# Performance work log

Measured on AMD Instinct MI355X. Metric: run time of the kernel, lower is better.

## Reference

```python
import jax, jax.numpy as jnp
import numpy as np
from jax import lax

B, NMEAS, M, LAYER_NUM = 2048, 128, 256, 10
CLAMP_MIN, CLAMP_MAX = 1e-6, 100.0
EPS_S = 1e-6


def _conv2d(x, w, b):
    y = lax.conv_general_dilated(x, w, (1, 1), 'SAME', dimension_numbers=('NCHW', 'OIHW', 'NCHW'))
    return y + b[None, :, None, None]


def _conv1d(x, w, b):
    y = lax.conv_general_dilated(x, w, (1,), 'SAME', dimension_numbers=('NCH', 'OIH', 'NCH'))
    return y + b[None, :, None]


def setup_inputs():
    key = jax.random.key(0)
    ks = jax.random.split(key, 12)
    s = 1.0 / np.sqrt(2.0 * NMEAS)  # ~unit-norm dictionary columns
    return {
        'Yr': jax.random.normal(ks[0], (B, 1, NMEAS, 1), jnp.float32),
        'Yi': jax.random.normal(ks[1], (B, 1, NMEAS, 1), jnp.float32),
        'Ar': s * jax.random.normal(ks[2], (NMEAS, M), jnp.float32),
        'Ai': s * jax.random.normal(ks[3], (NMEAS, M), jnp.float32),
        'conv1_w': 0.1 * jax.random.normal(ks[4], (32, 2, 3, 3), jnp.float32),
        'conv1_b': jnp.zeros((32,), jnp.float32),
        'conv2_w': 0.1 * jax.random.normal(ks[5], (64, 32, 3, 3), jnp.float32),
        'conv2_b': jnp.zeros((64,), jnp.float32),
        'hc_w': 0.1 * jax.random.normal(ks[6], (LAYER_NUM - 1, 64, 3), jnp.float32),
        'hc_b': jnp.zeros((LAYER_NUM - 1,), jnp.float32),
        'hd_w': 0.1 * jax.random.normal(ks[7], (LAYER_NUM - 1, 64, 3), jnp.float32),
        'hd_b': jnp.zeros((LAYER_NUM - 1,), jnp.float32),
        'hT_w': 0.1 * jax.random.normal(ks[8], (LAYER_NUM, 64, 3), jnp.float32),
        'hT_b': jnp.zeros((LAYER_NUM,), jnp.float32),
        'a0': jnp.asarray(1.0, jnp.float32),
        'b0': jnp.asarray(1.0, jnp.float32),
    }


def _hypernet(ay, c1w, c1b, c2w, c2b, hcw, hcb, hdw, hdb, hTw, hTb):
    # ay: [B, 2, M]; batch acts as image width (context)
    x_img = jnp.transpose(ay, (1, 2, 0))[None]              # [1, 2, M, B]
    f = jax.nn.relu(_conv2d(x_img, c1w, c1b))               # [1, 32, M, B]
    f = jax.nn.relu(_conv2d(f, c2w, c2b))                   # [1, 64, M, B]
    f = jnp.mean(f, axis=2)                                 # AdaptiveAvgPool2d((1,None)) -> [1, 64, B]
    c = jnp.abs(_conv1d(f, hcw, hcb))[0].T                  # [B, L-1]
    d = jnp.abs(_conv1d(f, hdw, hdb))[0].T                  # [B, L-1]
    T = jnp.abs(_conv1d(f, hTw, hTb))[0].T                  # [B, L]
    c = jnp.clip(c, CLAMP_MIN, CLAMP_MAX)
    d = jnp.maximum(d, CLAMP_MIN)
    T = jnp.clip(T, CLAMP_MIN, CLAMP_MAX)
    return c, d, T


def _forward(Yr, Yi, Ar, Ai, conv1_w, conv1_b, conv2_w, conv2_b,
             hc_w, hc_b, hd_w, hd_b, hT_w, hT_b, a0, b0):
    Y = (Yr + 1j * Yi).astype(jnp.complex64)                # [B,1,Nmeas,1]
    A = (Ar + 1j * Ai).astype(jnp.complex64)                # [Nmeas,M]
    AT = A.conj().T                                         # [M,Nmeas]
    AA = AT @ A                                             # [M,M] Hermitian
    AY = jnp.matmul(AT, Y)                                  # [B,1,M,1]
    b = Y.shape[0]
    n = Y.shape[2]
    ay = jnp.concatenate([AY.real.reshape(b, 1, -1), AY.imag.reshape(b, 1, -1)], axis=1)  # [B,2,M]
    c, d, T = _hypernet(ay, conv1_w, conv1_b, conv2_w, conv2_b,
                        hc_w, hc_b, hd_w, hd_b, hT_w, hT_b)
    D = jnp.real(jnp.diagonal(AA))[None, None, :, None]     # diag of Hermitian AA is real; [1,1,M,1]
    eps = (a0 / b0).astype(jnp.complex64) * jnp.ones((b, 1, 1, 1), jnp.complex64)
    Lam = ((c[:, 0] / d[:, 0])[:, None, None, None] * jnp.ones((1, 1, M, 1), jnp.float32)).astype(jnp.complex64)
    U = jnp.zeros((b, 1, M, 1), jnp.complex64)
    a = a0 + n
    for k in range(LAYER_NUM - 1):
        Tk = T[:, k][:, None, None, None]
        # fused SBL/VAMP mean update
        U = eps * (Tk * U - jnp.matmul(AA, U) + AY) / (eps * Tk + Lam + EPS_S)
        Sigma = 1.0 / (eps * D + Lam + EPS_S)
        r = Y - jnp.matmul(A, U)
        eps1 = jnp.sum(r.real ** 2 + r.imag ** 2, axis=(2, 3), keepdims=True)  # ||.||_F^2
        eps2 = jnp.sum(D * Sigma, axis=(2, 3), keepdims=True)
        eps = a / (b0 + eps1 + eps2 + EPS_S)
        Lam = (c[:, k][:, None, None, None] + 1.0) / (
            d[:, k][:, None, None, None] + jnp.abs(U) ** 2 + Sigma + EPS_S)
    Tk = T[:, LAYER_NUM - 1][:, None, None, None]
    U = eps * (Tk * U - jnp.matmul(AA, U) + AY) / (eps * Tk + Lam + EPS_S)
    Ua = jnp.abs(U)
    Ua = Ua / (jnp.max(Ua) + 1e-8)
    return Ua, c, d, T


def reference(Yr, Yi, Ar, Ai, conv1_w, conv1_b, conv2_w, conv2_b,
              hc_w, hc_b, hd_w, hd_b, hT_w, hT_b, a0, b0):
    Ua, c, d, T = _forward(Yr, Yi, Ar, Ai, conv1_w, conv1_b, conv2_w, conv2_b,
                           hc_w, hc_b, hd_w, hd_b, hT_w, hT_b, a0, b0)
    # original returns the last batch row of c/d/T (detached diagnostics)
    return Ua, c[-1:, :], d[-1:, :], T[-1:, :]
```

## Files before the change

### kernel.cpp

```cpp
#include <hip/hip_runtime.h>
#include <math.h>

#define B_N   2048
#define NM    128
#define M_N   256
#define LNUM  10
#define EPS_Sf 1e-6f

typedef _Float16 half8 __attribute__((ext_vector_type(8)));
typedef float floatx4 __attribute__((ext_vector_type(4)));

__device__ __forceinline__ float frcp(float x) { return __builtin_amdgcn_rcpf(x); }

static constexpr size_t o_AA  = 0;
static constexpr size_t o_D   = o_AA  + 131072;
static constexpr size_t o_yn  = o_D   + 256;
static constexpr size_t o_AY  = o_yn  + 2048;
static constexpr size_t o_AYt = o_AY  + 1048576;
static constexpr size_t o_w2t = o_AYt + 1048576;
static constexpr size_t o_z1  = o_w2t + 18432;
static constexpr size_t o_fp  = o_z1  + 16777216;
static constexpr size_t o_f   = o_fp  + 2097152;
static constexpr size_t o_c   = o_f   + 131072;
static constexpr size_t o_dd  = o_c   + 18432;
static constexpr size_t o_T   = o_dd  + 18432;
static constexpr size_t o_Ua  = o_T   + 20480;
static constexpr size_t o_gm  = o_Ua  + 524288;

__global__ void k_pre(const float* __restrict__ Ar, const float* __restrict__ Ai,
                      const float* __restrict__ Yr, const float* __restrict__ Yi,
                      const float* __restrict__ w2, float* __restrict__ ws) {
    __shared__ float sb[2048];
    int blk = blockIdx.x;
    int tid = threadIdx.x;
    if (blk < 256) {
        float* cr = sb; float* ci = sb + NM;
        int i = blk, j = tid;
        if (j < NM) { cr[j] = Ar[j * M_N + i]; ci[j] = Ai[j * M_N + i]; }
        __syncthreads();
        float sr = 0.f, si = 0.f;
        for (int n = 0; n < NM; ++n) {
            float ar = Ar[n * M_N + j], ai = Ai[n * M_N + j];
            sr += cr[n] * ar + ci[n] * ai;
            si += cr[n] * ai - ci[n] * ar;
        }
        _Float16* A16 = (_Float16*)(ws + o_AA);
        size_t off = ((size_t)((i >> 4) * 8 + (j >> 5)) * 64
                      + (size_t)(((j >> 3) & 3) * 16 + (i & 15))) * 8 + (j & 7);
        A16[off]         = (_Float16)sr;
        A16[65536 + off] = (_Float16)si;
        if (j == i) ws[o_D + i] = sr;
        if (i == 0 && j == 0) *(unsigned int*)(ws + o_gm) = 0u;
    } else if (blk < 328) {
        int i = (blk - 256) * 256 + tid;
        if (i < 64 * 32 * 9) {
            int oc = i / 288, r = i % 288;
            int ic = r / 9, kk = r % 9;
            _Float16* Wa = (_Float16*)(ws + o_w2t);
            Wa[((size_t)oc * 9 + kk) * 32 + ic] = (_Float16)w2[i];
        }
    } else {
        float2* Ys = (float2*)sb;
        int bb0 = (blk - 328) * 8;
        for (int i = tid; i < 8 * NM; i += 256) {
            int g = i >> 7, n = i & 127;
            Ys[g * NM + n] = make_float2(Yr[(size_t)(bb0 + g) * NM + n],
                                         Yi[(size_t)(bb0 + g) * NM + n]);
        }
        __syncthreads();
        if (tid < 8) {
            float s = 0.f;
            for (int n = 0; n < NM; ++n) { float2 y = Ys[tid * NM + n]; s += y.x * y.x + y.y * y.y; }
            ws[o_yn + bb0 + tid] = s;
        }
        int m = tid;
        float accr[8], acci[8];
#pragma unroll
        for (int g = 0; g < 8; ++g) { accr[g] = 0.f; acci[g] = 0.f; }
        for (int n = 0; n < NM; ++n) {
            float ar = Ar[n * M_N + m], ai = Ai[n * M_N + m];
#pragma unroll
            for (int g = 0; g < 8; ++g) {
                float2 y = Ys[g * NM + n];
                accr[g] += ar * y.x + ai * y.y;
                acci[g] += ar * y.y - ai * y.x;
            }
        }
        float2* AY = (float2*)(ws + o_AY);
#pragma unroll
        for (int g = 0; g < 8; ++g) {
            AY[(size_t)(bb0 + g) * M_N + m] = make_float2(accr[g], acci[g]);
            ws[o_AYt + (size_t)m * B_N + (bb0 + g)] = accr[g];
            ws[o_AYt + 524288 + (size_t)m * B_N + (bb0 + g)] = acci[g];
        }
    }
}

#define MFMA16(A,Bv,C) C = __builtin_amdgcn_mfma_f32_16x16x32_f16(A, Bv, C, 0, 0, 0)
__global__ void __launch_bounds__(256)
k_conv12(const float* __restrict__ w1, const float* __restrict__ b1,
         const float* __restrict__ b2, float* __restrict__ ws) {
    __shared__ __align__(16) _Float16 zt[18 * 18 * 40];
    int tid = threadIdx.x;
    int lane = tid & 63, w = tid >> 6;
    int col = lane & 15, quad = lane >> 4;
    int bt = blockIdx.x & 127, g = blockIdx.x >> 7;
    int b0 = bt * 16, m0 = g * 16;

    half8 Aw[2];
#pragma unroll
    for (int t = 0; t < 2; ++t)
#pragma unroll
        for (int j = 0; j < 8; ++j) {
            int k = quad * 8 + j;
            int oc = t * 16 + col;
            Aw[t][j] = (k < 18) ? (_Float16)w1[oc * 18 + (k & 1) * 9 + (k >> 1)]
                                : (_Float16)0.f;
        }
    float b1a[4], b1b[4];
#pragma unroll
    for (int r = 0; r < 4; ++r) { b1a[r] = b1[quad * 4 + r]; b1b[r] = b1[16 + quad * 4 + r]; }

    int dmj[8], dbj[8], offc[8];
#pragma unroll
    for (int j = 0; j < 8; ++j) {
        int k = quad * 8 + j;
        int e = k >> 1;
        int dm = (e * 11) >> 5;
        int db = e - dm * 3;
        if (k >= 18) dm = 1 << 20;
        dmj[j] = dm; dbj[j] = db;
        offc[j] = (k & 1) * 524288;
    }

    const float* xr = ws + o_AYt;
    for (int grp = w; grp < 21; grp += 4) {
        int p = grp * 16 + col;
        int mz = (p * 57) >> 10;
        int bz = p - mz * 18;
        int m_pt = m0 - 2 + mz, b_pt = b0 - 2 + bz;
        bool pok = (p < 324);
        half8 xb;
#pragma unroll
        for (int j = 0; j < 8; ++j) {
            int row = m_pt + dmj[j], bc = b_pt + dbj[j];
            bool ok = pok && ((unsigned)row < (unsigned)M_N) && ((unsigned)bc < (unsigned)B_N);
            float v = ok ? xr[(size_t)offc[j] + (size_t)row * B_N + bc] : 0.f;
            xb[j] = (_Float16)v;
        }
        floatx4 z0 = (floatx4){0.f, 0.f, 0.f, 0.f};
        floatx4 z1v = (floatx4){0.f, 0.f, 0.f, 0.f};
        MFMA16(Aw[0], xb, z0);
        MFMA16(Aw[1], xb, z1v);
        bool zok = ((unsigned)(m0 - 1 + mz) < (unsigned)M_N) &&
                   ((unsigned)(b0 - 1 + bz) < (unsigned)B_N);
        unsigned long long u0 = 0ull, u1 = 0ull;
        if (zok) {
            union { _Float16 h[4]; unsigned long long u; } a;
#pragma unroll
            for (int r = 0; r < 4; ++r) a.h[r] = (_Float16)fmaxf(z0[r] + b1a[r], 0.f);
            u0 = a.u;
#pragma unroll
            for (int r = 0; r < 4; ++r) a.h[r] = (_Float16)fmaxf(z1v[r] + b1b[r], 0.f);
            u1 = a.u;
        }
        if (pok) {
            _Float16* d = zt + (size_t)(mz * 18 + bz) * 40 + quad * 4;
            *(unsigned long long*)(d)      = u0;
            *(unsigned long long*)(d + 16) = u1;
        }
    }

    const _Float16* Wa = (const _Float16*)(ws + o_w2t);
    int oc0w = w * 16;
    half8 Af[9];
#pragma unroll
    for (int kk = 0; kk < 9; ++kk)
        Af[kk] = *(const half8*)(Wa + ((size_t)(oc0w + col) * 9 + kk) * 32 + quad * 8);
    float bias2[4];
#pragma unroll
    for (int r = 0; r < 4; ++r) bias2[r] = b2[oc0w + quad * 4 + r];

    __syncthreads();

    const _Float16* zb = zt + (size_t)col * 40 + (size_t)quad * 8;
    half8 Bf[3][3];
#pragma unroll
    for (int ph = 0; ph < 3; ++ph)
#pragma unroll
        for (int db = 0; db < 3; ++db)
            Bf[ph][db] = *(const half8*)(zb + (size_t)ph * 720 + (size_t)db * 40);

    floatx4 facc = (floatx4){0.f, 0.f, 0.f, 0.f};
#pragma unroll
    for (int mm = 0; mm < 16; ++mm) {
        floatx4 a0 = (floatx4){0.f, 0.f, 0.f, 0.f};
#pragma unroll
        for (int dm = 0; dm < 3; ++dm) {
            int ph = (mm + dm) % 3;
#pragma unroll
            for (int db = 0; db < 3; ++db)
                MFMA16(Af[dm * 3 + db], Bf[ph][db], a0);
        }
#pragma unroll
        for (int r = 0; r < 4; ++r) facc[r] += fmaxf(a0[r] + bias2[r], 0.f);
        if (mm < 15) {
            int ph = mm % 3;
#pragma unroll
            for (int db = 0; db < 3; ++db)
                Bf[ph][db] = *(const half8*)(zb + (size_t)(mm + 3) * 720 + (size_t)db * 40);
        }
    }
    float* fp = ws + o_fp + (size_t)g * 131072;
#pragma unroll
    for (int r = 0; r < 4; ++r)
        fp[(size_t)(oc0w + quad * 4 + r) * B_N + b0 + col] = facc[r];
}

__global__ void k_fred(float* __restrict__ ws) {
    size_t i = (size_t)blockIdx.x * 256 + threadIdx.x;
    float s = 0.f;
    for (int p = 0; p < 16; ++p) s += ws[o_fp + (size_t)p * 131072 + i];
    ws[o_f + i] = s * (1.f / 256.f);
}

__global__ void k_cdt(const float* __restrict__ hcw, const float* __restrict__ hcb,
                      const float* __restrict__ hdw, const float* __restrict__ hdb,
                      const float* __restrict__ hTw, const float* __restrict__ hTb,
                      float* __restrict__ ws, float* __restrict__ out) {
    int l = blockIdx.x >> 3;
    int b = (blockIdx.x & 7) * 256 + threadIdx.x;
    const float* f = ws + o_f;
    const float* w; float bi; int li, kind;
    if (l < 9)       { kind = 0; li = l;      w = hcw + (size_t)li * 192; bi = hcb[li]; }
    else if (l < 18) { kind = 1; li = l - 9;  w = hdw + (size_t)li * 192; bi = hdb[li]; }
    else             { kind = 2; li = l - 18; w = hTw + (size_t)li * 192; bi = hTb[li]; }
    __shared__ float wsm[192];
    for (int i = threadIdx.x; i < 192; i += 256) wsm[i] = w[i];
    __syncthreads();
    float acc = bi;
    bool okL = (b > 0), okR = (b < B_N - 1);
    for (int ic = 0; ic < 64; ++ic) {
        const float* fr = f + (size_t)ic * B_N + b;
        float fm1 = okL ? fr[-1] : 0.f;
        float f0  = fr[0];
        float fp1 = okR ? fr[1] : 0.f;
        acc += fm1 * wsm[ic * 3] + f0 * wsm[ic * 3 + 1] + fp1 * wsm[ic * 3 + 2];
    }
    float v = fmaxf(fabsf(acc), 1e-6f);
    if (kind != 1) v = fminf(v, 100.f);
    if (kind == 0)      { ws[o_c  + (size_t)b * 9  + li] = v; if (b == B_N - 1) out[524288 + li] = v; }
    else if (kind == 1) { ws[o_dd + (size_t)b * 9  + li] = v; if (b == B_N - 1) out[524297 + li] = v; }
    else                { ws[o_T  + (size_t)b * 10 + li] = v; if (b == B_N - 1) out[524306 + li] = v; }
}

__global__ void __launch_bounds__(512, 2)
k_iter(const float* __restrict__ a0p, const float* __restrict__ b0p, float* __restrict__ ws) {
    __shared__ __align__(16) _Float16 Ubf[2][8][64][8];
    __shared__ __align__(16) float redv[16][28];
    __shared__ float redm[8];
    int tid = threadIdx.x;
    int lane = tid & 63, w = tid >> 6;
    int col = lane & 15, quad = lane >> 4;
    int b = blockIdx.x * 16 + col;

    for (int i = tid; i < 16 * 28; i += 512) ((float*)redv)[i] = 0.f;

    const float2* AY = (const float2*)(ws + o_AY);
    const _Float16* Af = (const _Float16*)(ws + o_AA);
    float a0 = a0p[0], b0v = b0p[0];
    float atot = a0 + (float)NM;
    float yn = ws[o_yn + b];
    float eps = a0 / b0v;

    half8 Ar8[2][8], Ai8[2][8];
#pragma unroll
    for (int t = 0; t < 2; ++t)
#pragma unroll
        for (int ks = 0; ks < 8; ++ks) {
            const _Float16* ab = Af + (((size_t)(w * 2 + t) * 8 + ks) * 64 + lane) * 8;
            Ar8[t][ks] = *(const half8*)(ab);
            Ai8[t][ks] = *(const half8*)(ab + 65536);
        }

    float Dv[8], ayr[8], ayi[8], lam[8], Ur[8], Ui[8];
    float c0h = ws[o_c + (size_t)b * 9];
    float d0h = ws[o_dd + (size_t)b * 9];
    float T0 = ws[o_T + (size_t)b * 10];
    float lam0 = c0h * frcp(d0h);
#pragma unroll
    for (int ri = 0; ri < 8; ++ri) {
        int m = w * 32 + (ri >> 2) * 16 + quad * 4 + (ri & 3);
        Dv[ri] = ws[o_D + m];
        float2 a = AY[(size_t)b * M_N + m];
        ayr[ri] = a.x; ayi[ri] = a.y;
        lam[ri] = lam0;
    }
    {
        float iv = eps * frcp(fmaf(eps, T0, lam0 + EPS_Sf));
#pragma unroll
        for (int ri = 0; ri < 8; ++ri) { Ur[ri] = iv * ayr[ri]; Ui[ri] = iv * ayi[ri]; }
    }

    int laneD0 = ((quad >> 1)) * 16 + col;
    int laneD1 = (2 + (quad >> 1)) * 16 + col;
    int eb = (quad & 1) * 4;

    for (int k = 0; k < LNUM - 1; ++k) {
        float ck = ws[o_c + (size_t)b * 9 + k];
        float dk = ws[o_dd + (size_t)b * 9 + k];
        float Tn = ws[o_T + (size_t)b * 10 + k + 1];
        {
            union { _Float16 h[4]; unsigned long long u; } pk;
#pragma unroll
            for (int t = 0; t < 2; ++t) {
                int ld = t ? laneD1 : laneD0;
#pragma unroll
                for (int r = 0; r < 4; ++r) pk.h[r] = (_Float16)Ur[t * 4 + r];
                *(unsigned long long*)&Ubf[0][w][ld][eb] = pk.u;
#pragma unroll
                for (int r = 0; r < 4; ++r) pk.h[r] = (_Float16)Ui[t * 4 + r];
                *(unsigned long long*)&Ubf[1][w][ld][eb] = pk.u;
            }
        }
        __syncthreads();
        floatx4 ac[8];
#pragma unroll
        for (int i = 0; i < 8; ++i) ac[i] = (floatx4){0.f, 0.f, 0.f, 0.f};
#pragma unroll
        for (int ks = 0; ks < 8; ++ks) {
            half8 urh = *(const half8*)&Ubf[0][ks][lane][0];
            half8 uih = *(const half8*)&Ubf[1][ks][lane][0];
            MFMA16(Ar8[0][ks], urh, ac[0]);
            MFMA16(Ai8[0][ks], uih, ac[1]);
            MFMA16(Ar8[0][ks], uih, ac[2]);
            MFMA16(Ai8[0][ks], urh, ac[3]);
            MFMA16(Ar8[1][ks], urh, ac[4]);
            MFMA16(Ai8[1][ks], uih, ac[5]);
            MFMA16(Ar8[1][ks], uih, ac[6]);
            MFMA16(Ai8[1][ks], urh, ac[7]);
        }
        float wr[8], wi[8], sg[8];
        float p1 = 0.f, p2 = 0.f, p3 = 0.f;
#pragma unroll
        for (int t = 0; t < 2; ++t)
#pragma unroll
            for (int r = 0; r < 4; ++r) {
                int ri = t * 4 + r;
                wr[ri] = ac[t * 4 + 0][r] - ac[t * 4 + 1][r];
                wi[ri] = ac[t * 4 + 2][r] + ac[t * 4 + 3][r];
                sg[ri] = frcp(fmaf(eps, Dv[ri], lam[ri] + EPS_Sf));
                p1 += ayr[ri] * Ur[ri] + ayi[ri] * Ui[ri];
                p2 += Ur[ri] * wr[ri] + Ui[ri] * wi[ri];
                p3 += Dv[ri] * sg[ri];
            }
        p1 += __shfl_xor(p1, 16); p1 += __shfl_xor(p1, 32);
        p2 += __shfl_xor(p2, 16); p2 += __shfl_xor(p2, 32);
        p3 += __shfl_xor(p3, 16); p3 += __shfl_xor(p3, 32);
        if (lane < 16) {
            redv[col][w * 3]     = p1;
            redv[col][w * 3 + 1] = p2;
            redv[col][w * 3 + 2] = p3;
        }
        __syncthreads();
        float s[3] = {0.f, 0.f, 0.f};
#pragma unroll
        for (int j = 0; j < 7; ++j) {
            floatx4 v4 = *(const floatx4*)&redv[col][j * 4];
#pragma unroll
            for (int e = 0; e < 4; ++e) s[(j * 4 + e) % 3] += v4[e];
        }
        float eps1 = fmaxf(yn - 2.f * s[0] + s[1], 0.f);
        eps = atot * frcp(b0v + eps1 + s[2] + EPS_Sf);
        float ck1 = ck + 1.f;
#pragma unroll
        for (int ri = 0; ri < 8; ++ri) {
            lam[ri] = ck1 * frcp(dk + Ur[ri] * Ur[ri] + Ui[ri] * Ui[ri] + sg[ri] + EPS_Sf);
            float iv = eps * frcp(fmaf(eps, Tn, lam[ri] + EPS_Sf));
            Ur[ri] = iv * (Tn * Ur[ri] - wr[ri] + ayr[ri]);
            Ui[ri] = iv * (Tn * Ui[ri] - wi[ri] + ayi[ri]);
        }
    }
    float lm = 0.f;
#pragma unroll
    for (int t = 0; t < 2; ++t) {
        float4 v;
        v.x = sqrtf(Ur[t * 4 + 0] * Ur[t * 4 + 0] + Ui[t * 4 + 0] * Ui[t * 4 + 0]);
        v.y = sqrtf(Ur[t * 4 + 1] * Ur[t * 4 + 1] + Ui[t * 4 + 1] * Ui[t * 4 + 1]);
        v.z = sqrtf(Ur[t * 4 + 2] * Ur[t * 4 + 2] + Ui[t * 4 + 2] * Ui[t * 4 + 2]);
        v.w = sqrtf(Ur[t * 4 + 3] * Ur[t * 4 + 3] + Ui[t * 4 + 3] * Ui[t * 4 + 3]);
        *(float4*)&ws[o_Ua + (size_t)b * M_N + w * 32 + t * 16 + quad * 4] = v;
        lm = fmaxf(lm, fmaxf(fmaxf(v.x, v.y), fmaxf(v.z, v.w)));
    }
#pragma unroll
    for (int off = 32; off >= 1; off >>= 1) lm = fmaxf(lm, __shfl_xor(lm, off));
    if (lane == 0) redm[w] = lm;
    __syncthreads();
    if (tid == 0) {
        float mx = redm[0];
#pragma unroll
        for (int i = 1; i < 8; ++i) mx = fmaxf(mx, redm[i]);
        atomicMax((unsigned int*)(ws + o_gm), __float_as_uint(mx));
    }
}

__global__ void k_norm(const float* __restrict__ ws, float* __restrict__ out) {
    size_t i = (size_t)blockIdx.x * 256 + threadIdx.x;
    float gm = __uint_as_float(*(const unsigned int*)(ws + o_gm));
    out[i] = ws[o_Ua + i] / (gm + 1e-8f);
}

extern "C" void kernel_launch(void* const* d_in, const int* in_sizes, int n_in,
                              void* d_out, int out_size, void* d_ws, size_t ws_size,
                              hipStream_t stream) {
    (void)in_sizes; (void)n_in; (void)out_size; (void)ws_size;
    const float* Yr  = (const float*)d_in[0];
    const float* Yi  = (const float*)d_in[1];
    const float* Ar  = (const float*)d_in[2];
    const float* Ai  = (const float*)d_in[3];
    const float* w1  = (const float*)d_in[4];
    const float* b1  = (const float*)d_in[5];
    const float* w2  = (const float*)d_in[6];
    const float* b2  = (const float*)d_in[7];
    const float* hcw = (const float*)d_in[8];
    const float* hcb = (const float*)d_in[9];
    const float* hdw = (const float*)d_in[10];
    const float* hdb = (const float*)d_in[11];
    const float* hTw = (const float*)d_in[12];
    const float* hTb = (const float*)d_in[13];
    const float* a0  = (const float*)d_in[14];
    const float* b0  = (const float*)d_in[15];
    float* ws = (float*)d_ws;
    float* out = (float*)d_out;

    k_pre   <<<584, 256, 0, stream>>>(Ar, Ai, Yr, Yi, w2, ws);
    k_conv12<<<2048, 256, 0, stream>>>(w1, b1, b2, ws);
    k_fred  <<<512, 256, 0, stream>>>(ws);
    k_cdt   <<<224, 256, 0, stream>>>(hcw, hcb, hdw, hdb, hTw, hTb, ws, out);
    k_iter  <<<128, 512, 0, stream>>>(a0, b0, ws);
    k_norm  <<<2048, 256, 0, stream>>>(ws, out);
}
```

Before: 231.3 us.

## Fuse mean reduction into conv via atomics and stage conv1 input tile in LDS

The conv1+conv2 kernel now accumulates its per-tile partial sums straight into the pooled feature buffer with atomicAdd, so the separate reduction kernel and the 16-slice partial buffer go away. The 1/256 mean scaling moves into the hypernet conv weights, and the pre-kernel gets extra blocks to zero the buffer. The conv1 input patch is loaded cooperatively once into shared memory as fp16 instead of each lane gathering from global memory, and the zt stride changes to 44 to avoid bank conflicts. Atomics add contention and a non-deterministic summation order.

```diff
diff --git a/kernel.cpp b/kernel.cpp
--- a/kernel.cpp
+++ b/kernel.cpp
@@ -59,7 +59,7 @@
             _Float16* Wa = (_Float16*)(ws + o_w2t);
             Wa[((size_t)oc * 9 + kk) * 32 + ic] = (_Float16)w2[i];
         }
-    } else {
+    } else if (blk < 584) {
         float2* Ys = (float2*)sb;
         int bb0 = (blk - 328) * 8;
         for (int i = tid; i < 8 * NM; i += 256) {
@@ -93,6 +93,9 @@
             ws[o_AYt + (size_t)m * B_N + (bb0 + g)] = accr[g];
             ws[o_AYt + 524288 + (size_t)m * B_N + (bb0 + g)] = acci[g];
         }
+    } else {
+        size_t idx = (size_t)(blk - 584) * 1024 + (size_t)tid * 4;
+        *(float4*)(ws + o_f + idx) = make_float4(0.f, 0.f, 0.f, 0.f);
     }
 }
 
@@ -100,13 +103,24 @@
 __global__ void __launch_bounds__(256)
 k_conv12(const float* __restrict__ w1, const float* __restrict__ b1,
          const float* __restrict__ b2, float* __restrict__ ws) {
-    __shared__ __align__(16) _Float16 zt[18 * 18 * 40];
+    __shared__ __align__(16) _Float16 zt[324 * 44];
+    __shared__ __align__(16) _Float16 xsf[800];
     int tid = threadIdx.x;
     int lane = tid & 63, w = tid >> 6;
     int col = lane & 15, quad = lane >> 4;
     int bt = blockIdx.x & 127, g = blockIdx.x >> 7;
     int b0 = bt * 16, m0 = g * 16;
 
+    const _Float16* Wa = (const _Float16*)(ws + o_w2t);
+    int oc0w = w * 16;
+    half8 Af[9];
+#pragma unroll
+    for (int kk = 0; kk < 9; ++kk)
+        Af[kk] = *(const half8*)(Wa + ((size_t)(oc0w + col) * 9 + kk) * 32 + quad * 8);
+    float bias2[4];
+#pragma unroll
+    for (int r = 0; r < 4; ++r) bias2[r] = b2[oc0w + quad * 4 + r];
+
     half8 Aw[2];
 #pragma unroll
     for (int t = 0; t < 2; ++t)
@@ -121,33 +135,39 @@
 #pragma unroll
     for (int r = 0; r < 4; ++r) { b1a[r] = b1[quad * 4 + r]; b1b[r] = b1[16 + quad * 4 + r]; }
 
-    int dmj[8], dbj[8], offc[8];
+    int basej[8];
 #pragma unroll
     for (int j = 0; j < 8; ++j) {
         int k = quad * 8 + j;
-        int e = k >> 1;
+        int c = k & 1, e = k >> 1;
         int dm = (e * 11) >> 5;
         int db = e - dm * 3;
-        if (k >= 18) dm = 1 << 20;
-        dmj[j] = dm; dbj[j] = db;
-        offc[j] = (k & 1) * 524288;
+        basej[j] = (k < 18) ? (c * 400 + dm * 20 + db) : 0;
     }
 
     const float* xr = ws + o_AYt;
+    for (int i = tid; i < 800; i += 256) {
+        int c = (i >= 400) ? 1 : 0;
+        int rem = i - c * 400;
+        int r = (rem * 205) >> 12;
+        int q = rem - r * 20;
+        int row = m0 - 2 + r, bc = b0 - 2 + q;
+        float v = (((unsigned)row < (unsigned)M_N) && ((unsigned)bc < (unsigned)B_N))
+                    ? xr[(size_t)c * 524288 + (size_t)row * B_N + bc] : 0.f;
+        xsf[i] = (_Float16)v;
+    }
+    __syncthreads();
+
     for (int grp = w; grp < 21; grp += 4) {
         int p = grp * 16 + col;
+        bool pok = (p < 324);
         int mz = (p * 57) >> 10;
         int bz = p - mz * 18;
-        int m_pt = m0 - 2 + mz, b_pt = b0 - 2 + bz;
-        bool pok = (p < 324);
+        if (!pok) { mz = 0; bz = 0; }
+        int base = mz * 20 + bz;
         half8 xb;
 #pragma unroll
-        for (int j = 0; j < 8; ++j) {
-            int row = m_pt + dmj[j], bc = b_pt + dbj[j];
-            bool ok = pok && ((unsigned)row < (unsigned)M_N) && ((unsigned)bc < (unsigned)B_N);
-            float v = ok ? xr[(size_t)offc[j] + (size_t)row * B_N + bc] : 0.f;
-            xb[j] = (_Float16)v;
-        }
+        for (int j = 0; j < 8; ++j) xb[j] = xsf[basej[j] + base];
         floatx4 z0 = (floatx4){0.f, 0.f, 0.f, 0.f};
         floatx4 z1v = (floatx4){0.f, 0.f, 0.f, 0.f};
         MFMA16(Aw[0], xb, z0);
@@ -165,31 +185,20 @@
             u1 = a.u;
         }
         if (pok) {
-            _Float16* d = zt + (size_t)(mz * 18 + bz) * 40 + quad * 4;
+            _Float16* d = zt + (size_t)p * 44 + quad * 4;
             *(unsigned long long*)(d)      = u0;
             *(unsigned long long*)(d + 16) = u1;
         }
     }
-
-    const _Float16* Wa = (const _Float16*)(ws + o_w2t);
-    int oc0w = w * 16;
-    half8 Af[9];
-#pragma unroll
-    for (int kk = 0; kk < 9; ++kk)
-        Af[kk] = *(const half8*)(Wa + ((size_t)(oc0w + col) * 9 + kk) * 32 + quad * 8);
-    float bias2[4];
-#pragma unroll
-    for (int r = 0; r < 4; ++r) bias2[r] = b2[oc0w + quad * 4 + r];
-
     __syncthreads();
 
-    const _Float16* zb = zt + (size_t)col * 40 + (size_t)quad * 8;
+    const _Float16* zb = zt + (size_t)col * 44 + (size_t)quad * 8;
     half8 Bf[3][3];
 #pragma unroll
     for (int ph = 0; ph < 3; ++ph)
 #pragma unroll
         for (int db = 0; db < 3; ++db)
-            Bf[ph][db] = *(const half8*)(zb + (size_t)ph * 720 + (size_t)db * 40);
+            Bf[ph][db] = *(const half8*)(zb + (size_t)ph * 792 + (size_t)db * 44);
 
     floatx4 facc = (floatx4){0.f, 0.f, 0.f, 0.f};
 #pragma unroll
@@ -208,20 +217,13 @@
             int ph = mm % 3;
 #pragma unroll
             for (int db = 0; db < 3; ++db)
-                Bf[ph][db] = *(const half8*)(zb + (size_t)(mm + 3) * 720 + (size_t)db * 40);
-        }
-    }
-    float* fp = ws + o_fp + (size_t)g * 131072;
+                Bf[ph][db] = *(const half8*)(zb + (size_t)(mm + 3) * 792 + (size_t)db * 44);
+        }
+    }
+    float* f = ws + o_f;
 #pragma unroll
     for (int r = 0; r < 4; ++r)
-        fp[(size_t)(oc0w + quad * 4 + r) * B_N + b0 + col] = facc[r];
-}
-
-__global__ void k_fred(float* __restrict__ ws) {
-    size_t i = (size_t)blockIdx.x * 256 + threadIdx.x;
-    float s = 0.f;
-    for (int p = 0; p < 16; ++p) s += ws[o_fp + (size_t)p * 131072 + i];
-    ws[o_f + i] = s * (1.f / 256.f);
+        atomicAdd(&f[(size_t)(oc0w + quad * 4 + r) * B_N + b0 + col], facc[r]);
 }
 
 __global__ void k_cdt(const float* __restrict__ hcw, const float* __restrict__ hcb,
@@ -236,7 +238,7 @@
     else if (l < 18) { kind = 1; li = l - 9;  w = hdw + (size_t)li * 192; bi = hdb[li]; }
     else             { kind = 2; li = l - 18; w = hTw + (size_t)li * 192; bi = hTb[li]; }
     __shared__ float wsm[192];
-    for (int i = threadIdx.x; i < 192; i += 256) wsm[i] = w[i];
+    for (int i = threadIdx.x; i < 192; i += 256) wsm[i] = w[i] * (1.f / 256.f);
     __syncthreads();
     float acc = bi;
     bool okL = (b > 0), okR = (b < B_N - 1);
@@ -433,9 +435,8 @@
     float* ws = (float*)d_ws;
     float* out = (float*)d_out;
 
-    k_pre   <<<584, 256, 0, stream>>>(Ar, Ai, Yr, Yi, w2, ws);
+    k_pre   <<<712, 256, 0, stream>>>(Ar, Ai, Yr, Yi, w2, ws);
     k_conv12<<<2048, 256, 0, stream>>>(w1, b1, b2, ws);
-    k_fred  <<<512, 256, 0, stream>>>(ws);
     k_cdt   <<<224, 256, 0, stream>>>(hcw, hcb, hdw, hdb, hTw, hTb, ws, out);
     k_iter  <<<128, 512, 0, stream>>>(a0, b0, ws);
     k_norm  <<<2048, 256, 0, stream>>>(ws, out);
```

Result: no change. 233.5 us (+0.9%).

## Fuse pooling reduction, hypernet heads and normalization into conv and iteration kernels

Applied to the files above, without the earlier changes.

Conv12 now accumulates its per-row-tile pooled features straight into a zeroed buffer with atomicAdd, which removes the 16-way partial buffer and the k_fred reduction kernel. The c/d/T 1D conv heads are computed per block inside k_iter into shared memory, so k_cdt goes away. The final max-normalization moves into k_iter through a grid-wide atomic counter spin barrier, which removes k_norm and the Ua round trip. The LDS row padding changes from 40 to 44 to avoid bank conflicts. Costs include float-atomic contention, non-deterministic summation order, a spin barrier that relies on all 128 blocks being co-resident, and head conv work repeated per block.

```diff
diff --git a/kernel.cpp b/kernel.cpp
--- a/kernel.cpp
+++ b/kernel.cpp
@@ -18,14 +18,9 @@
 static constexpr size_t o_AY  = o_yn  + 2048;
 static constexpr size_t o_AYt = o_AY  + 1048576;
 static constexpr size_t o_w2t = o_AYt + 1048576;
-static constexpr size_t o_z1  = o_w2t + 18432;
-static constexpr size_t o_fp  = o_z1  + 16777216;
-static constexpr size_t o_f   = o_fp  + 2097152;
-static constexpr size_t o_c   = o_f   + 131072;
-static constexpr size_t o_dd  = o_c   + 18432;
-static constexpr size_t o_T   = o_dd  + 18432;
-static constexpr size_t o_Ua  = o_T   + 20480;
-static constexpr size_t o_gm  = o_Ua  + 524288;
+static constexpr size_t o_cnt = o_w2t + 18432;
+static constexpr size_t o_f   = o_cnt + 1024;
+static constexpr size_t o_gm  = o_f   + 131072;
 
 __global__ void k_pre(const float* __restrict__ Ar, const float* __restrict__ Ai,
                       const float* __restrict__ Yr, const float* __restrict__ Yi,
@@ -50,7 +45,10 @@
         A16[off]         = (_Float16)sr;
         A16[65536 + off] = (_Float16)si;
         if (j == i) ws[o_D + i] = sr;
-        if (i == 0 && j == 0) *(unsigned int*)(ws + o_gm) = 0u;
+        if (i == 0 && j == 0) {
+            *(unsigned int*)(ws + o_gm) = 0u;
+            *(unsigned int*)(ws + o_cnt) = 0u;
+        }
     } else if (blk < 328) {
         int i = (blk - 256) * 256 + tid;
         if (i < 64 * 32 * 9) {
@@ -59,7 +57,7 @@
             _Float16* Wa = (_Float16*)(ws + o_w2t);
             Wa[((size_t)oc * 9 + kk) * 32 + ic] = (_Float16)w2[i];
         }
-    } else {
+    } else if (blk < 584) {
         float2* Ys = (float2*)sb;
         int bb0 = (blk - 328) * 8;
         for (int i = tid; i < 8 * NM; i += 256) {
@@ -93,19 +91,33 @@
             ws[o_AYt + (size_t)m * B_N + (bb0 + g)] = accr[g];
             ws[o_AYt + 524288 + (size_t)m * B_N + (bb0 + g)] = acci[g];
         }
+    } else {
+        size_t idx = (size_t)(blk - 584) * 1024 + (size_t)tid * 4;
+        *(float4*)(ws + o_f + idx) = make_float4(0.f, 0.f, 0.f, 0.f);
     }
 }
 
 #define MFMA16(A,Bv,C) C = __builtin_amdgcn_mfma_f32_16x16x32_f16(A, Bv, C, 0, 0, 0)
+
 __global__ void __launch_bounds__(256)
 k_conv12(const float* __restrict__ w1, const float* __restrict__ b1,
          const float* __restrict__ b2, float* __restrict__ ws) {
-    __shared__ __align__(16) _Float16 zt[18 * 18 * 40];
+    __shared__ __align__(16) _Float16 zt[324 * 44];
     int tid = threadIdx.x;
     int lane = tid & 63, w = tid >> 6;
     int col = lane & 15, quad = lane >> 4;
     int bt = blockIdx.x & 127, g = blockIdx.x >> 7;
     int b0 = bt * 16, m0 = g * 16;
+
+    const _Float16* Wa = (const _Float16*)(ws + o_w2t);
+    int oc0w = w * 16;
+    half8 Af[9];
+#pragma unroll
+    for (int kk = 0; kk < 9; ++kk)
+        Af[kk] = *(const half8*)(Wa + ((size_t)(oc0w + col) * 9 + kk) * 32 + quad * 8);
+    float bias2[4];
+#pragma unroll
+    for (int r = 0; r < 4; ++r) bias2[r] = b2[oc0w + quad * 4 + r];
 
     half8 Aw[2];
 #pragma unroll
@@ -165,31 +177,20 @@
             u1 = a.u;
         }
         if (pok) {
-            _Float16* d = zt + (size_t)(mz * 18 + bz) * 40 + quad * 4;
+            _Float16* d = zt + (size_t)p * 44 + quad * 4;
             *(unsigned long long*)(d)      = u0;
             *(unsigned long long*)(d + 16) = u1;
         }
     }
-
-    const _Float16* Wa = (const _Float16*)(ws + o_w2t);
-    int oc0w = w * 16;
-    half8 Af[9];
-#pragma unroll
-    for (int kk = 0; kk < 9; ++kk)
-        Af[kk] = *(const half8*)(Wa + ((size_t)(oc0w + col) * 9 + kk) * 32 + quad * 8);
-    float bias2[4];
-#pragma unroll
-    for (int r = 0; r < 4; ++r) bias2[r] = b2[oc0w + quad * 4 + r];
-
     __syncthreads();
 
-    const _Float16* zb = zt + (size_t)col * 40 + (size_t)quad * 8;
+    const _Float16* zb = zt + (size_t)col * 44 + (size_t)quad * 8;
     half8 Bf[3][3];
 #pragma unroll
     for (int ph = 0; ph < 3; ++ph)
 #pragma unroll
         for (int db = 0; db < 3; ++db)
-            Bf[ph][db] = *(const half8*)(zb + (size_t)ph * 720 + (size_t)db * 40);
+            Bf[ph][db] = *(const half8*)(zb + (size_t)ph * 792 + (size_t)db * 44);
 
     floatx4 facc = (floatx4){0.f, 0.f, 0.f, 0.f};
 #pragma unroll
@@ -208,63 +209,55 @@
             int ph = mm % 3;
 #pragma unroll
             for (int db = 0; db < 3; ++db)
-                Bf[ph][db] = *(const half8*)(zb + (size_t)(mm + 3) * 720 + (size_t)db * 40);
-        }
-    }
-    float* fp = ws + o_fp + (size_t)g * 131072;
+                Bf[ph][db] = *(const half8*)(zb + (size_t)(mm + 3) * 792 + (size_t)db * 44);
+        }
+    }
+    float* f = ws + o_f;
 #pragma unroll
     for (int r = 0; r < 4; ++r)
-        fp[(size_t)(oc0w + quad * 4 + r) * B_N + b0 + col] = facc[r];
+        atomicAdd(&f[(size_t)(oc0w + quad * 4 + r) * B_N + b0 + col], facc[r]);
 }
 
-__global__ void k_fred(float* __restrict__ ws) {
-    size_t i = (size_t)blockIdx.x * 256 + threadIdx.x;
-    float s = 0.f;
-    for (int p = 0; p < 16; ++p) s += ws[o_fp + (size_t)p * 131072 + i];
-    ws[o_f + i] = s * (1.f / 256.f);
-}
-
-__global__ void k_cdt(const float* __restrict__ hcw, const float* __restrict__ hcb,
-                      const float* __restrict__ hdw, const float* __restrict__ hdb,
-                      const float* __restrict__ hTw, const float* __restrict__ hTb,
-                      float* __restrict__ ws, float* __restrict__ out) {
-    int l = blockIdx.x >> 3;
-    int b = (blockIdx.x & 7) * 256 + threadIdx.x;
-    const float* f = ws + o_f;
-    const float* w; float bi; int li, kind;
-    if (l < 9)       { kind = 0; li = l;      w = hcw + (size_t)li * 192; bi = hcb[li]; }
-    else if (l < 18) { kind = 1; li = l - 9;  w = hdw + (size_t)li * 192; bi = hdb[li]; }
-    else             { kind = 2; li = l - 18; w = hTw + (size_t)li * 192; bi = hTb[li]; }
-    __shared__ float wsm[192];
-    for (int i = threadIdx.x; i < 192; i += 256) wsm[i] = w[i];
-    __syncthreads();
-    float acc = bi;
-    bool okL = (b > 0), okR = (b < B_N - 1);
-    for (int ic = 0; ic < 64; ++ic) {
-        const float* fr = f + (size_t)ic * B_N + b;
-        float fm1 = okL ? fr[-1] : 0.f;
-        float f0  = fr[0];
-        float fp1 = okR ? fr[1] : 0.f;
-        acc += fm1 * wsm[ic * 3] + f0 * wsm[ic * 3 + 1] + fp1 * wsm[ic * 3 + 2];
-    }
-    float v = fmaxf(fabsf(acc), 1e-6f);
-    if (kind != 1) v = fminf(v, 100.f);
-    if (kind == 0)      { ws[o_c  + (size_t)b * 9  + li] = v; if (b == B_N - 1) out[524288 + li] = v; }
-    else if (kind == 1) { ws[o_dd + (size_t)b * 9  + li] = v; if (b == B_N - 1) out[524297 + li] = v; }
-    else                { ws[o_T  + (size_t)b * 10 + li] = v; if (b == B_N - 1) out[524306 + li] = v; }
-}
-
 __global__ void __launch_bounds__(512, 2)
-k_iter(const float* __restrict__ a0p, const float* __restrict__ b0p, float* __restrict__ ws) {
+k_iter(const float* __restrict__ a0p, const float* __restrict__ b0p,
+       const float* __restrict__ hcw, const float* __restrict__ hcb,
+       const float* __restrict__ hdw, const float* __restrict__ hdb,
+       const float* __restrict__ hTw, const float* __restrict__ hTb,
+       float* __restrict__ ws, float* __restrict__ out) {
     __shared__ __align__(16) _Float16 Ubf[2][8][64][8];
     __shared__ __align__(16) float redv[16][28];
     __shared__ float redm[8];
+    __shared__ float cC[16][9], cD[16][9], cT[16][10];
     int tid = threadIdx.x;
     int lane = tid & 63, w = tid >> 6;
     int col = lane & 15, quad = lane >> 4;
     int b = blockIdx.x * 16 + col;
 
     for (int i = tid; i < 16 * 28; i += 512) ((float*)redv)[i] = 0.f;
+
+    if (tid < 448) {
+        int l = tid >> 4, colp = tid & 15;
+        int bb = blockIdx.x * 16 + colp;
+        const float* fbase = ws + o_f;
+        const float* wv_; float bi; int li, kind;
+        if (l < 9)       { kind = 0; li = l;      wv_ = hcw + (size_t)li * 192; bi = hcb[li]; }
+        else if (l < 18) { kind = 1; li = l - 9;  wv_ = hdw + (size_t)li * 192; bi = hdb[li]; }
+        else             { kind = 2; li = l - 18; wv_ = hTw + (size_t)li * 192; bi = hTb[li]; }
+        float s = 0.f;
+        bool okL = (bb > 0), okR = (bb < B_N - 1);
+        for (int ic = 0; ic < 64; ++ic) {
+            const float* fr = fbase + (size_t)ic * B_N + bb;
+            float fm1 = okL ? fr[-1] : 0.f;
+            float f0  = fr[0];
+            float fp1 = okR ? fr[1] : 0.f;
+            s += fm1 * wv_[ic * 3] + f0 * wv_[ic * 3 + 1] + fp1 * wv_[ic * 3 + 2];
+        }
+        float v = fmaxf(fabsf(bi + s * (1.f / 256.f)), 1e-6f);
+        if (kind != 1) v = fminf(v, 100.f);
+        if (kind == 0)      { cC[colp][li] = v; if (bb == B_N - 1) out[524288 + li] = v; }
+        else if (kind == 1) { cD[colp][li] = v; if (bb == B_N - 1) out[524297 + li] = v; }
+        else                { cT[colp][li] = v; if (bb == B_N - 1) out[524306 + li] = v; }
+    }
 
     const float2* AY = (const float2*)(ws + o_AY);
     const _Float16* Af = (const _Float16*)(ws + o_AA);
@@ -284,18 +277,18 @@
         }
 
     float Dv[8], ayr[8], ayi[8], lam[8], Ur[8], Ui[8];
-    float c0h = ws[o_c + (size_t)b * 9];
-    float d0h = ws[o_dd + (size_t)b * 9];
-    float T0 = ws[o_T + (size_t)b * 10];
-    float lam0 = c0h * frcp(d0h);
 #pragma unroll
     for (int ri = 0; ri < 8; ++ri) {
         int m = w * 32 + (ri >> 2) * 16 + quad * 4 + (ri & 3);
         Dv[ri] = ws[o_D + m];
         float2 a = AY[(size_t)b * M_N + m];
         ayr[ri] = a.x; ayi[ri] = a.y;
-        lam[ri] = lam0;
-    }
+    }
+    __syncthreads();
+    float lam0 = cC[col][0] * frcp(cD[col][0]);
+    float T0 = cT[col][0];
+#pragma unroll
+    for (int ri = 0; ri < 8; ++ri) lam[ri] = lam0;
     {
         float iv = eps * frcp(fmaf(eps, T0, lam0 + EPS_Sf));
 #pragma unroll
@@ -307,9 +300,9 @@
     int eb = (quad & 1) * 4;
 
     for (int k = 0; k < LNUM - 1; ++k) {
-        float ck = ws[o_c + (size_t)b * 9 + k];
-        float dk = ws[o_dd + (size_t)b * 9 + k];
-        float Tn = ws[o_T + (size_t)b * 10 + k + 1];
+        float ck = cC[col][k];
+        float dk = cD[col][k];
+        float Tn = cT[col][k + 1];
         {
             union { _Float16 h[4]; unsigned long long u; } pk;
 #pragma unroll
@@ -381,6 +374,7 @@
             Ui[ri] = iv * (Tn * Ui[ri] - wi[ri] + ayi[ri]);
         }
     }
+    float4 va[2];
     float lm = 0.f;
 #pragma unroll
     for (int t = 0; t < 2; ++t) {
@@ -389,25 +383,36 @@
         v.y = sqrtf(Ur[t * 4 + 1] * Ur[t * 4 + 1] + Ui[t * 4 + 1] * Ui[t * 4 + 1]);
         v.z = sqrtf(Ur[t * 4 + 2] * Ur[t * 4 + 2] + Ui[t * 4 + 2] * Ui[t * 4 + 2]);
         v.w = sqrtf(Ur[t * 4 + 3] * Ur[t * 4 + 3] + Ui[t * 4 + 3] * Ui[t * 4 + 3]);
-        *(float4*)&ws[o_Ua + (size_t)b * M_N + w * 32 + t * 16 + quad * 4] = v;
+        va[t] = v;
         lm = fmaxf(lm, fmaxf(fmaxf(v.x, v.y), fmaxf(v.z, v.w)));
     }
 #pragma unroll
     for (int off = 32; off >= 1; off >>= 1) lm = fmaxf(lm, __shfl_xor(lm, off));
     if (lane == 0) redm[w] = lm;
     __syncthreads();
+    unsigned int* gmp = (unsigned int*)(ws + o_gm);
+    unsigned int* cnt = (unsigned int*)(ws + o_cnt);
     if (tid == 0) {
         float mx = redm[0];
 #pragma unroll
         for (int i = 1; i < 8; ++i) mx = fmaxf(mx, redm[i]);
-        atomicMax((unsigned int*)(ws + o_gm), __float_as_uint(mx));
-    }
-}
-
-__global__ void k_norm(const float* __restrict__ ws, float* __restrict__ out) {
-    size_t i = (size_t)blockIdx.x * 256 + threadIdx.x;
-    float gm = __uint_as_float(*(const unsigned int*)(ws + o_gm));
-    out[i] = ws[o_Ua + i] / (gm + 1e-8f);
+        atomicMax(gmp, __float_as_uint(mx));
+        __threadfence();
+        __hip_atomic_fetch_add(cnt, 1u, __ATOMIC_ACQ_REL, __HIP_MEMORY_SCOPE_AGENT);
+        while (__hip_atomic_load(cnt, __ATOMIC_ACQUIRE, __HIP_MEMORY_SCOPE_AGENT) < gridDim.x)
+            __builtin_amdgcn_s_sleep(8);
+        redm[0] = __uint_as_float(
+            __hip_atomic_load(gmp, __ATOMIC_RELAXED, __HIP_MEMORY_SCOPE_AGENT));
+    }
+    __syncthreads();
+    float gm = redm[0];
+    float inv = 1.f / (gm + 1e-8f);
+#pragma unroll
+    for (int t = 0; t < 2; ++t) {
+        float4 v = va[t];
+        v.x *= inv; v.y *= inv; v.z *= inv; v.w *= inv;
+        *(float4*)&out[(size_t)b * M_N + w * 32 + t * 16 + quad * 4] = v;
+    }
 }
 
 extern "C" void kernel_launch(void* const* d_in, const int* in_sizes, int n_in,
@@ -433,10 +438,7 @@
     float* ws = (float*)d_ws;
     float* out = (float*)d_out;
 
-    k_pre   <<<584, 256, 0, stream>>>(Ar, Ai, Yr, Yi, w2, ws);
+    k_pre   <<<712, 256, 0, stream>>>(Ar, Ai, Yr, Yi, w2, ws);
     k_conv12<<<2048, 256, 0, stream>>>(w1, b1, b2, ws);
-    k_fred  <<<512, 256, 0, stream>>>(ws);
-    k_cdt   <<<224, 256, 0, stream>>>(hcw, hcb, hdw, hdb, hTw, hTb, ws, out);
-    k_iter  <<<128, 512, 0, stream>>>(a0, b0, ws);
-    k_norm  <<<2048, 256, 0, stream>>>(ws, out);
+    k_iter  <<<128, 512, 0, stream>>>(a0, b0, hcw, hcb, hdw, hdb, hTw, hTb, ws, out);
 }
```

New measurement: 259.3 us. 1.12x slower.
